# Kernel tuning notes

Hardware: AMD Instinct MI355X
Metric: run time of the kernel (lower is better)

Reference implementation:

```python
import jax, jax.numpy as jnp
import numpy as np
from math import sqrt


def _build_transitions(dim):
    # Upper-triangular (i<=j) pairs in the same row-major order as the torch loop.
    iu0, iu1 = np.triu_indices(dim)
    n_mono = len(iu0)
    idx = np.arange(n_mono)
    M = np.zeros((dim, dim), dtype=np.int32)
    M[iu0, iu1] = idx
    M[iu1, iu0] = idx
    coef_trans = np.full((n_mono, 1), sqrt(2.0), dtype=np.float32)
    coef_trans[idx[iu0 == iu1]] = 1.0  # diagonal coefficients stay scale 1
    return iu0, iu1, M.reshape(-1), coef_trans


def setup_inputs() -> dict:
    key = jax.random.key(0)
    k1, k2, k3, k4 = jax.random.split(key, 4)
    dim, n_quadrics, B = 512, 64, 2048
    n_mono = dim * (dim - 1) // 2 + dim  # 131328
    points = jax.random.normal(k1, (B, dim), dtype=jnp.float32)
    # orthogonal-ish init is only an init detail; random normal keeps math identical
    q_coefs = jax.random.normal(k2, (n_mono, n_quadrics), dtype=jnp.float32) / np.sqrt(n_mono)
    l_coefs = 2.0 * jax.random.uniform(k3, (dim, n_quadrics), dtype=jnp.float32) - 1.0
    free_coefs = 2.0 * jax.random.uniform(k4, (1, n_quadrics), dtype=jnp.float32) - 1.0
    return {"points": points, "q_coefs": q_coefs, "l_coefs": l_coefs, "free_coefs": free_coefs}


def reference(points, q_coefs, l_coefs, free_coefs):
    B, dim = points.shape
    nq = q_coefs.shape[1]
    iu0, iu1, inds_trans, coef_trans_np = _build_transitions(dim)
    coef_trans = jnp.asarray(coef_trans_np)

    # quadratic monomials: q[b, k] = p[b, i_k] * p[b, j_k]  (upper-tri order)
    q = points[:, iu0] * points[:, iu1]  # (B, n_mono)

    coefs = q_coefs * coef_trans  # (n_mono, nq) real coefficients

    # values of quadrics at points
    values = jnp.abs(q @ coefs + points @ l_coefs + free_coefs)  # (B, nq)

    # symmetric full matrices gathered from flat coefficient vector
    m_full = coefs[inds_trans].reshape(dim, dim, nq)  # (dim, dim, nq)
    dm = (jnp.eye(dim, dtype=points.dtype) + 1.0)[:, :, None]  # 2 on diag, ... wait: eye+ones -> 2 diag, 1 off
    m_scaled = m_full * dm

    # gradients: grad[b, k, e] = sum_d p[b, d] * m_scaled[d, e, k] + l_coefs[e, k]
    q_grad = jnp.einsum("bd,dek->bke", points, m_scaled) + l_coefs.T[None, :, :]  # (B, nq, dim)
    grad = jnp.sum(q_grad * q_grad, axis=2)  # (B, nq)

    norm = jnp.linalg.norm(q_coefs, axis=0)  # (nq,)
    scores = (jnp.sqrt(grad / 4.0 + values * norm) - jnp.sqrt(grad) / 2.0) / norm
    return scores
```

## Files before the change

kernel.cpp:

```cpp
#include <hip/hip_runtime.h>

#define DIM 512
#define NQ 64
#define BATCH 2048

typedef __bf16  bf16x8  __attribute__((ext_vector_type(8)));
typedef float   floatx4 __attribute__((ext_vector_type(4)));

static __device__ inline unsigned short f2bf(float f) {
    unsigned int u = __float_as_uint(f);
    return (unsigned short)((u + 0x7fffu + ((u >> 16) & 1u)) >> 16);
}
static __device__ inline float bf2f(unsigned short h) {
    return __uint_as_float((unsigned int)h << 16);
}
static __device__ inline unsigned int pack2(float a, float b) {
    return (unsigned)f2bf(a) | ((unsigned)f2bf(b) << 16);
}

__global__ void hsq_pack_kernel(const float* __restrict__ pts,
                                unsigned short* __restrict__ Pb) {
    const int i8 = blockIdx.x * 256 + threadIdx.x;
    const float4 v1 = *(const float4*)(pts + (size_t)i8 * 8);
    const float4 v2 = *(const float4*)(pts + (size_t)i8 * 8 + 4);
    uint4 wv;
    wv.x = pack2(v1.x, v1.y); wv.y = pack2(v1.z, v1.w);
    wv.z = pack2(v2.x, v2.y); wv.w = pack2(v2.z, v2.w);
    *(uint4*)(Pb + (size_t)i8 * 8) = wv;
}

__global__ __launch_bounds__(256, 4)
void hsq_expand_kernel(const float* __restrict__ qc,
                       unsigned short* __restrict__ W,
                       float* __restrict__ npart) {
    const int e    = blockIdx.x;
    const int dblk = blockIdx.y;
    const int pb   = blockIdx.y * 512 + blockIdx.x;
    const int wid  = threadIdx.x >> 6;
    const int k    = threadIdx.x & 63;
    const int d0   = dblk * 128 + wid * 32;

    __shared__ unsigned short tv[64 * 136];
    __shared__ float part[4][64];

    float v[32];
#pragma unroll
    for (int s = 0; s < 32; ++s) {
        const int d = d0 + s;
        const int i = d < e ? d : e;
        const int j = d < e ? e : d;
        const int idx = i * DIM - ((i * (i - 1)) >> 1) + (j - i);
        v[s] = qc[(size_t)idx * NQ + k];
    }

    float nacc = 0.0f;
#pragma unroll
    for (int s = 0; s < 32; ++s)
        if (d0 + s >= e) nacc += v[s] * v[s];

#pragma unroll
    for (int t = 0; t < 4; ++t) {
        float sc[8];
#pragma unroll
        for (int q = 0; q < 8; ++q) {
            const int d = d0 + t * 8 + q;
            sc[q] = v[t * 8 + q] * ((d == e) ? 2.0f : 1.41421356237309515f);
        }
        uint4 w;
        w.x = pack2(sc[0], sc[1]); w.y = pack2(sc[2], sc[3]);
        w.z = pack2(sc[4], sc[5]); w.w = pack2(sc[6], sc[7]);
        *(uint4*)&tv[k * 136 + wid * 32 + t * 8] = w;
    }
    part[wid][k] = nacc;
    __syncthreads();

#pragma unroll
    for (int r = 0; r < 4; ++r) {
        const int kk = r * 16 + (threadIdx.x >> 4);
        const int u  = threadIdx.x & 15;
        const uint4 w = *(const uint4*)&tv[kk * 136 + u * 8];
        *(uint4*)(W + ((size_t)(kk * DIM + e)) * DIM + dblk * 128 + u * 8) = w;
    }
    if (threadIdx.x < 64) {
        npart[(size_t)k * 2048 + pb] =
            part[0][k] + part[1][k] + part[2][k] + part[3][k];
    }
}

__global__ __launch_bounds__(256, 3)
void hsq_gemm_kernel(const unsigned short* __restrict__ Pb,
                     const unsigned short* __restrict__ W,
                     const float* __restrict__ l_coefs,
                     float2* __restrict__ part) {
    const int bid = blockIdx.x;
    const int xcd = bid & 7;
    const int loc = bid >> 3;
    const int k   = xcd * 8 + (loc >> 6);
    const int rem = loc & 63;
    const int eb  = rem >> 4;
    const int m0  = (rem & 15) * 128;

    const int tid   = threadIdx.x;
    const int w     = tid >> 6;
    const int lane  = tid & 63;
    const int mhalf = w >> 1, nhalf = w & 1;
    const int c     = lane & 15;
    const int quad  = lane >> 4;

    __shared__ unsigned short Ab[2][128 * 32];
    __shared__ unsigned short Bb[2][128 * 32];
    __shared__ float red[2][128][2];

    const unsigned short* Wk = W + (size_t)k * DIM * DIM + (size_t)eb * 128 * DIM;

#define STAGE(buf_, it_) do {                                                   \
    const int lr_  = lane >> 2;                                                 \
    const int gch_ = (lane & 3) ^ ((lane >> 3) & 3);                            \
    _Pragma("unroll")                                                           \
    for (int i_ = 0; i_ < 2; ++i_) {                                            \
        const int rb_  = w * 32 + i_ * 16;                                      \
        const int row_ = rb_ + lr_;                                             \
        __builtin_amdgcn_global_load_lds(                                       \
            (const __attribute__((address_space(1))) unsigned int*)             \
                (Pb + (size_t)(m0 + row_) * DIM + (it_) * 32 + gch_ * 8),       \
            (__attribute__((address_space(3))) unsigned int*)                   \
                &Ab[buf_][rb_ * 32], 16, 0, 0);                                 \
        __builtin_amdgcn_global_load_lds(                                       \
            (const __attribute__((address_space(1))) unsigned int*)             \
                (Wk + (size_t)row_ * DIM + (it_) * 32 + gch_ * 8),              \
            (__attribute__((address_space(3))) unsigned int*)                   \
                &Bb[buf_][rb_ * 32], 16, 0, 0);                                 \
    }                                                                           \
} while (0)

    floatx4 acc[4][4];
#pragma unroll
    for (int mt = 0; mt < 4; ++mt)
#pragma unroll
        for (int nt = 0; nt < 4; ++nt)
            acc[mt][nt] = (floatx4){0.f, 0.f, 0.f, 0.f};

    STAGE(0, 0);
    __syncthreads();

    for (int it = 0; it < 16; ++it) {
        const int buf = it & 1;
        if (it < 15) STAGE(buf ^ 1, it + 1);

        bf16x8 af[4], bfr[4];
#pragma unroll
        for (int mt = 0; mt < 4; ++mt) {
            const int row  = mhalf * 64 + mt * 16 + c;
            const int slot = quad ^ ((row >> 1) & 3);
            af[mt] = *(const bf16x8*)&Ab[buf][row * 32 + slot * 8];
        }
#pragma unroll
        for (int nt = 0; nt < 4; ++nt) {
            const int er   = nhalf * 64 + nt * 16 + c;
            const int slot = quad ^ ((er >> 1) & 3);
            bfr[nt] = *(const bf16x8*)&Bb[buf][er * 32 + slot * 8];
        }
#pragma unroll
        for (int mt = 0; mt < 4; ++mt)
#pragma unroll
            for (int nt = 0; nt < 4; ++nt)
                acc[mt][nt] = __builtin_amdgcn_mfma_f32_16x16x32_bf16(
                    af[mt], bfr[nt], acc[mt][nt], 0, 0, 0);
        __syncthreads();
    }
#undef STAGE

    float lcv[4];
#pragma unroll
    for (int nt = 0; nt < 4; ++nt)
        lcv[nt] = l_coefs[(eb * 128 + nhalf * 64 + nt * 16 + c) * NQ + k];

    const unsigned short* Pe = Pb + (size_t)(m0 + mhalf * 64) * DIM
                                  + eb * 128 + nhalf * 64 + c;
#pragma unroll
    for (int mt = 0; mt < 4; ++mt)
#pragma unroll
        for (int r = 0; r < 4; ++r) {
            const unsigned short* Prow = Pe + (size_t)(mt * 16 + quad * 4 + r) * DIM;
            float pv = 0.f, pg = 0.f;
#pragma unroll
            for (int nt = 0; nt < 4; ++nt) {
                const float g = acc[mt][nt][r];
                const float l = lcv[nt];
                pv += bf2f(Prow[nt * 16]) * (0.5f * g + l);
                const float gq = g + l;
                pg += gq * gq;
            }
#pragma unroll
            for (int off = 1; off < 16; off <<= 1) {
                pv += __shfl_xor(pv, off);
                pg += __shfl_xor(pg, off);
            }
            if (c == 0) {
                const int row = mhalf * 64 + mt * 16 + quad * 4 + r;
                red[nhalf][row][0] = pv;
                red[nhalf][row][1] = pg;
            }
        }
    __syncthreads();

    if (tid < 128) {
        const float pv = red[0][tid][0] + red[1][tid][0];
        const float pg = red[0][tid][1] + red[1][tid][1];
        part[((size_t)(eb * NQ + k)) * BATCH + m0 + tid] = make_float2(pv, pg);
    }
}

__global__ void hsq_final_kernel(const float2* __restrict__ part,
                                 const float* __restrict__ npart,
                                 const float* __restrict__ free_coefs,
                                 float* __restrict__ out) {
    const int k = blockIdx.x;
    const int t = threadIdx.x;
    __shared__ float ws[4];

    const float4* src = (const float4*)(npart + (size_t)k * 2048);
    const float4 a = src[t * 2], b = src[t * 2 + 1];
    float s = a.x + a.y + a.z + a.w + b.x + b.y + b.z + b.w;
#pragma unroll
    for (int off = 1; off < 64; off <<= 1) s += __shfl_xor(s, off);
    if ((t & 63) == 0) ws[t >> 6] = s;
    __syncthreads();
    const float nrm = sqrtf(ws[0] + ws[1] + ws[2] + ws[3]);
    const float fc  = free_coefs[k];

#pragma unroll
    for (int i = 0; i < 8; ++i) {
        const int bidx = i * 256 + t;
        float pv = 0.f, pg = 0.f;
#pragma unroll
        for (int eb = 0; eb < 4; ++eb) {
            const float2 p = part[((size_t)(eb * NQ + k)) * BATCH + bidx];
            pv += p.x; pg += p.y;
        }
        const float vals = fabsf(pv + fc);
        out[(size_t)bidx * NQ + k] = (sqrtf(0.25f * pg + vals * nrm) - 0.5f * sqrtf(pg)) / nrm;
    }
}

extern "C" void kernel_launch(void* const* d_in, const int* in_sizes, int n_in,
                              void* d_out, int out_size, void* d_ws, size_t ws_size,
                              hipStream_t stream) {
    const float* points     = (const float*)d_in[0];
    const float* q_coefs    = (const float*)d_in[1];
    const float* l_coefs    = (const float*)d_in[2];
    const float* free_coefs = (const float*)d_in[3];
    float* out = (float*)d_out;

    char* ws = (char*)d_ws;
    unsigned short* W  = (unsigned short*)ws;
    unsigned short* Pb = (unsigned short*)(ws + 33554432);
    float2*         part  = (float2*)(ws + 35651584);
    float*          npart = (float*)(ws + 39845888);

    hsq_pack_kernel<<<dim3(BATCH * DIM / 8 / 256), 256, 0, stream>>>(points, Pb);
    hsq_expand_kernel<<<dim3(DIM, 4), 256, 0, stream>>>(q_coefs, W, npart);
    hsq_gemm_kernel<<<dim3(NQ * 64), 256, 0, stream>>>(Pb, W, l_coefs, part);
    hsq_final_kernel<<<dim3(NQ), 256, 0, stream>>>(part, npart, free_coefs, out);
}
```

Measured before the change: 204.8 us.

## Give each wave private LDS tiles and drop block barriers in GEMM loop

The GEMM main loop now has each wave stage its own 64-row A and B slices into a private LDS region, instead of sharing block-wide tiles. This removes the per-iteration __syncthreads. The loop is unrolled by two with both buffers prefetched up front, and launch bounds drop to 2 blocks per CU to fit the larger 64 KB LDS footprint. In exchange, A and B rows are fetched redundantly by pairs of waves, which doubles global/L2 traffic. Correctness also relies on the compiler inserting vmcnt waits before LDS reads of the async loads.

Measured after the change: 229.2 us. 1.12x slower.

```diff
diff --git a/kernel.cpp b/kernel.cpp
--- a/kernel.cpp
+++ b/kernel.cpp
@@ -87,7 +87,7 @@
     }
 }
 
-__global__ __launch_bounds__(256, 3)
+__global__ __launch_bounds__(256, 2)
 void hsq_gemm_kernel(const unsigned short* __restrict__ Pb,
                      const unsigned short* __restrict__ W,
                      const float* __restrict__ l_coefs,
@@ -107,32 +107,56 @@
     const int c     = lane & 15;
     const int quad  = lane >> 4;
 
-    __shared__ unsigned short Ab[2][128 * 32];
-    __shared__ unsigned short Bb[2][128 * 32];
+    __shared__ unsigned short S[4 * 8192];
     __shared__ float red[2][128][2];
 
-    const unsigned short* Wk = W + (size_t)k * DIM * DIM + (size_t)eb * 128 * DIM;
+    unsigned short* Sw = S + w * 8192;
+    const unsigned short* PA = Pb + (size_t)(m0 + mhalf * 64) * DIM;
+    const unsigned short* WB = W + (size_t)k * DIM * DIM
+                                 + (size_t)(eb * 128 + nhalf * 64) * DIM;
+
+    const int lr  = lane >> 2;
+    const int gch = (lane & 3) ^ ((lr >> 1) & 3);
 
 #define STAGE(buf_, it_) do {                                                   \
-    const int lr_  = lane >> 2;                                                 \
-    const int gch_ = (lane & 3) ^ ((lane >> 3) & 3);                            \
-    _Pragma("unroll")                                                           \
-    for (int i_ = 0; i_ < 2; ++i_) {                                            \
-        const int rb_  = w * 32 + i_ * 16;                                      \
-        const int row_ = rb_ + lr_;                                             \
+    _Pragma("unroll")                                                           \
+    for (int i_ = 0; i_ < 4; ++i_) {                                            \
+        const int rl_ = i_ * 16 + lr;                                           \
         __builtin_amdgcn_global_load_lds(                                       \
             (const __attribute__((address_space(1))) unsigned int*)             \
-                (Pb + (size_t)(m0 + row_) * DIM + (it_) * 32 + gch_ * 8),       \
+                (PA + (size_t)rl_ * DIM + (it_) * 32 + gch * 8),                \
             (__attribute__((address_space(3))) unsigned int*)                   \
-                &Ab[buf_][rb_ * 32], 16, 0, 0);                                 \
+                (Sw + (buf_) * 2048 + i_ * 512), 16, 0, 0);                     \
         __builtin_amdgcn_global_load_lds(                                       \
             (const __attribute__((address_space(1))) unsigned int*)             \
-                (Wk + (size_t)row_ * DIM + (it_) * 32 + gch_ * 8),              \
+                (WB + (size_t)rl_ * DIM + (it_) * 32 + gch * 8),                \
             (__attribute__((address_space(3))) unsigned int*)                   \
-                &Bb[buf_][rb_ * 32], 16, 0, 0);                                 \
+                (Sw + 4096 + (buf_) * 2048 + i_ * 512), 16, 0, 0);              \
     }                                                                           \
 } while (0)
 
+#define COMPUTE(buf_) do {                                                      \
+    bf16x8 af[4], bfr[4];                                                       \
+    _Pragma("unroll")                                                           \
+    for (int mt = 0; mt < 4; ++mt) {                                            \
+        const int row  = mt * 16 + c;                                           \
+        const int slot = quad ^ ((row >> 1) & 3);                               \
+        af[mt] = *(const bf16x8*)&Sw[(buf_) * 2048 + row * 32 + slot * 8];      \
+    }                                                                           \
+    _Pragma("unroll")                                                           \
+    for (int nt = 0; nt < 4; ++nt) {                                            \
+        const int er   = nt * 16 + c;                                           \
+        const int slot = quad ^ ((er >> 1) & 3);                                \
+        bfr[nt] = *(const bf16x8*)&Sw[4096 + (buf_) * 2048 + er * 32 + slot * 8]; \
+    }                                                                           \
+    _Pragma("unroll")                                                           \
+    for (int mt = 0; mt < 4; ++mt)                                              \
+        _Pragma("unroll")                                                       \
+        for (int nt = 0; nt < 4; ++nt)                                          \
+            acc[mt][nt] = __builtin_amdgcn_mfma_f32_16x16x32_bf16(              \
+                af[mt], bfr[nt], acc[mt][nt], 0, 0, 0);                         \
+} while (0)
+
     floatx4 acc[4][4];
 #pragma unroll
     for (int mt = 0; mt < 4; ++mt)
@@ -141,34 +165,17 @@
             acc[mt][nt] = (floatx4){0.f, 0.f, 0.f, 0.f};
 
     STAGE(0, 0);
-    __syncthreads();
-
-    for (int it = 0; it < 16; ++it) {
-        const int buf = it & 1;
-        if (it < 15) STAGE(buf ^ 1, it + 1);
-
-        bf16x8 af[4], bfr[4];
-#pragma unroll
-        for (int mt = 0; mt < 4; ++mt) {
-            const int row  = mhalf * 64 + mt * 16 + c;
-            const int slot = quad ^ ((row >> 1) & 3);
-            af[mt] = *(const bf16x8*)&Ab[buf][row * 32 + slot * 8];
-        }
-#pragma unroll
-        for (int nt = 0; nt < 4; ++nt) {
-            const int er   = nhalf * 64 + nt * 16 + c;
-            const int slot = quad ^ ((er >> 1) & 3);
-            bfr[nt] = *(const bf16x8*)&Bb[buf][er * 32 + slot * 8];
-        }
-#pragma unroll
-        for (int mt = 0; mt < 4; ++mt)
-#pragma unroll
-            for (int nt = 0; nt < 4; ++nt)
-                acc[mt][nt] = __builtin_amdgcn_mfma_f32_16x16x32_bf16(
-                    af[mt], bfr[nt], acc[mt][nt], 0, 0, 0);
-        __syncthreads();
-    }
+    STAGE(1, 1);
+    for (int h = 0; h < 7; ++h) {
+        COMPUTE(0);
+        STAGE(0, 2 * h + 2);
+        COMPUTE(1);
+        STAGE(1, 2 * h + 3);
+    }
+    COMPUTE(0);
+    COMPUTE(1);
 #undef STAGE
+#undef COMPUTE
 
     float lcv[4];
 #pragma unroll
```

## Load B operand directly from global into registers instead of LDS staging

Applied to the files above, without the earlier changes.

The main GEMM kernel stops staging the W (B operand) tile through shared memory. Each lane now loads its bf16x8 fragments straight from global memory into registers, double-buffered one iteration ahead. This removes half of the LDS traffic and its footprint, which may raise occupancy. The cost is uncoalesced, strided global reads and higher register pressure. The launch_bounds hint on the expand kernel is also dropped.

Measured after the change: 259.1 us. +26.6%, slower.

```diff
diff --git a/kernel.cpp b/kernel.cpp
--- a/kernel.cpp
+++ b/kernel.cpp
@@ -29,7 +29,7 @@
     *(uint4*)(Pb + (size_t)i8 * 8) = wv;
 }
 
-__global__ __launch_bounds__(256, 4)
+__global__
 void hsq_expand_kernel(const float* __restrict__ qc,
                        unsigned short* __restrict__ W,
                        float* __restrict__ npart) {
@@ -108,7 +108,6 @@
     const int quad  = lane >> 4;
 
     __shared__ unsigned short Ab[2][128 * 32];
-    __shared__ unsigned short Bb[2][128 * 32];
     __shared__ float red[2][128][2];
 
     const unsigned short* Wk = W + (size_t)k * DIM * DIM + (size_t)eb * 128 * DIM;
@@ -125,14 +124,17 @@
                 (Pb + (size_t)(m0 + row_) * DIM + (it_) * 32 + gch_ * 8),       \
             (__attribute__((address_space(3))) unsigned int*)                   \
                 &Ab[buf_][rb_ * 32], 16, 0, 0);                                 \
-        __builtin_amdgcn_global_load_lds(                                       \
-            (const __attribute__((address_space(1))) unsigned int*)             \
-                (Wk + (size_t)row_ * DIM + (it_) * 32 + gch_ * 8),              \
-            (__attribute__((address_space(3))) unsigned int*)                   \
-                &Bb[buf_][rb_ * 32], 16, 0, 0);                                 \
     }                                                                           \
 } while (0)
 
+    const unsigned short* Wb = Wk + (size_t)(nhalf * 64 + c) * DIM + quad * 8;
+
+#define LOADB(dst_, it_) do {                                                   \
+    _Pragma("unroll")                                                           \
+    for (int nt = 0; nt < 4; ++nt)                                              \
+        dst_[nt] = *(const bf16x8*)(Wb + (size_t)nt * 16 * DIM + (it_) * 32);   \
+} while (0)
+
     floatx4 acc[4][4];
 #pragma unroll
     for (int mt = 0; mt < 4; ++mt)
@@ -140,14 +142,20 @@
         for (int nt = 0; nt < 4; ++nt)
             acc[mt][nt] = (floatx4){0.f, 0.f, 0.f, 0.f};
 
+    bf16x8 bcur[4], bnext[4];
     STAGE(0, 0);
-    __syncthreads();
-
+    LOADB(bcur, 0);
+    __syncthreads();
+
+#pragma unroll 2
     for (int it = 0; it < 16; ++it) {
         const int buf = it & 1;
-        if (it < 15) STAGE(buf ^ 1, it + 1);
-
-        bf16x8 af[4], bfr[4];
+        if (it < 15) {
+            STAGE(buf ^ 1, it + 1);
+            LOADB(bnext, it + 1);
+        }
+
+        bf16x8 af[4];
 #pragma unroll
         for (int mt = 0; mt < 4; ++mt) {
             const int row  = mhalf * 64 + mt * 16 + c;
@@ -155,20 +163,18 @@
             af[mt] = *(const bf16x8*)&Ab[buf][row * 32 + slot * 8];
         }
 #pragma unroll
-        for (int nt = 0; nt < 4; ++nt) {
-            const int er   = nhalf * 64 + nt * 16 + c;
-            const int slot = quad ^ ((er >> 1) & 3);
-            bfr[nt] = *(const bf16x8*)&Bb[buf][er * 32 + slot * 8];
-        }
-#pragma unroll
         for (int mt = 0; mt < 4; ++mt)
 #pragma unroll
             for (int nt = 0; nt < 4; ++nt)
                 acc[mt][nt] = __builtin_amdgcn_mfma_f32_16x16x32_bf16(
-                    af[mt], bfr[nt], acc[mt][nt], 0, 0, 0);
+                    af[mt], bcur[nt], acc[mt][nt], 0, 0, 0);
+
+#pragma unroll
+        for (int nt = 0; nt < 4; ++nt) bcur[nt] = bnext[nt];
         __syncthreads();
     }
 #undef STAGE
+#undef LOADB
 
     float lcv[4];
 #pragma unroll
```
